# Performance work log

Hardware: AMD Instinct MI355X
Metric: run time of the kernel (lower is better)

The kernel has to match this reference:

```python
import jax, jax.numpy as jnp
import numpy as np

H = 256            # hidden_size
N_NODE = 50000     # item vocab
NUM_GRAPHS = 4096
NODES_PER_G = 20
EDGES_PER_G = 40
N = NUM_GRAPHS * NODES_PER_G      # 81920
E = NUM_GRAPHS * EDGES_PER_G      # 163840


def setup_inputs() -> dict:
    key = jax.random.key(0)
    ks = jax.random.split(key, 16)
    stdv = 1.0 / np.sqrt(H)
    u = lambda k, shape: jax.random.uniform(k, shape, jnp.float32, -stdv, stdv)

    # graph data: 1-based item ids, sorted batch vector, within-graph edges
    x = jax.random.randint(ks[0], (N,), 1, N_NODE, dtype=jnp.int64)
    batch = jnp.repeat(jnp.arange(NUM_GRAPHS, dtype=jnp.int64), NODES_PER_G)
    base = jnp.repeat(jnp.arange(NUM_GRAPHS, dtype=jnp.int64) * NODES_PER_G, EDGES_PER_G)
    src = base + jax.random.randint(ks[1], (E,), 0, NODES_PER_G, dtype=jnp.int64)
    dst = base + jax.random.randint(ks[2], (E,), 0, NODES_PER_G, dtype=jnp.int64)
    edge_index = jnp.stack([src, dst])

    return {
        "x": x, "edge_index": edge_index, "batch": batch,
        "emb": u(ks[3], (N_NODE, H)),
        "gated_w": u(ks[4], (2, H, H)),      # GatedGraphConv weight, num_layers=2
        "w_ih": u(ks[5], (3 * H, H)), "w_hh": u(ks[6], (3 * H, H)),
        "b_ih": u(ks[7], (3 * H,)), "b_hh": u(ks[8], (3 * H,)),
        "W1": u(ks[9], (H, H)), "b1": u(ks[10], (H,)),
        "W2": u(ks[11], (H, H)), "b2": u(ks[12], (H,)),
        "qw": u(ks[13], (1, H)), "qb": u(ks[14], (1,)),
        "W3": u(ks[15], (H, 2 * H)), "b3": jnp.zeros((H,), jnp.float32),
    }


def _forward(x, edge_index, batch, emb, gated_w, w_ih, w_hh, b_ih, b_hh,
             W1, b1, W2, b2, qw, qb, W3, b3):
    h = emb[x - 1]                                   # [N, H] embedding lookup
    src, dst = edge_index[0], edge_index[1]

    # GatedGraphConv: 2 layers of (linear -> scatter-add over edges -> GRUCell)
    for i in range(2):
        m = h @ gated_w[i]                           # [N, H]
        agg = jnp.zeros_like(h).at[dst].add(m[src])  # message aggregation
        gi = agg @ w_ih.T + b_ih                     # GRU input gates
        gh = h @ w_hh.T + b_hh                       # GRU hidden gates
        i_r, i_z, i_n = jnp.split(gi, 3, axis=-1)
        h_r, h_z, h_n = jnp.split(gh, 3, axis=-1)
        r = jax.nn.sigmoid(i_r + h_r)
        z = jax.nn.sigmoid(i_z + h_z)
        n = jnp.tanh(i_n + r * h_n)
        h = (1.0 - z) * n + z * h

    # Embedding2Score: last-node attention readout per graph
    counts = jnp.bincount(batch, length=NUM_GRAPHS)          # [B]
    last_idx = jnp.cumsum(counts) - 1                        # last node of each graph
    v_n = h[last_idx]                                        # [B, H]
    alpha = jax.nn.sigmoid(v_n[batch] @ W1.T + b1 + h @ W2.T + b2) @ qw.T + qb  # [N, 1]
    s_g = jax.ops.segment_sum(alpha * h, batch, num_segments=NUM_GRAPHS)        # [B, H]
    s_h = jnp.concatenate([v_n, s_g], axis=-1) @ W3.T + b3                      # [B, H]
    return s_h @ emb.T                                       # [B, N_NODE] scores


def reference(x, edge_index, batch, emb, gated_w, w_ih, w_hh, b_ih, b_hh,
              W1, b1, W2, b2, qw, qb, W3, b3):
    return _forward(x, edge_index, batch, emb, gated_w, w_ih, w_hh, b_ih, b_hh,
                    W1, b1, W2, b2, qw, qb, W3, b3)
```

## Files before the change

### kernel.cpp

```cpp
#include <hip/hip_runtime.h>

typedef __attribute__((ext_vector_type(8))) __bf16 bf16x8;
typedef __attribute__((ext_vector_type(4))) float f32x4;

#define DEV __device__ __forceinline__

DEV unsigned short f2bf(float f) {
  unsigned u = __float_as_uint(f);
  u = (u + 0x7fffu + ((u >> 16) & 1u)) >> 16;
  return (unsigned short)u;
}
DEV float bf2f(unsigned short s) { return __uint_as_float(((unsigned)s) << 16); }
DEV float sigm(float x) { return 1.f / (1.f + expf(-x)); }

DEV uint4 pack8(f32x4 a, f32x4 b) {
  uint4 o;
  o.x = (unsigned)f2bf(a[0]) | ((unsigned)f2bf(a[1]) << 16);
  o.y = (unsigned)f2bf(a[2]) | ((unsigned)f2bf(a[3]) << 16);
  o.z = (unsigned)f2bf(b[0]) | ((unsigned)f2bf(b[1]) << 16);
  o.w = (unsigned)f2bf(b[2]) | ((unsigned)f2bf(b[3]) << 16);
  return o;
}

#define GL16(SRC, LDSB)                                                                    \
  __builtin_amdgcn_global_load_lds(                                                       \
      (const __attribute__((address_space(1))) unsigned int*)(SRC),                       \
      (__attribute__((address_space(3))) unsigned int*)(LDSB), 16, 0, 0)

template<int MODE, bool BIAS>
__global__ __launch_bounds__(256)
void gemm_bt(const unsigned short* __restrict__ A, const unsigned short* __restrict__ Bm,
             const float* __restrict__ bias, void* __restrict__ Cv,
             const float* __restrict__ vw1, const float* __restrict__ qwf,
             const int* __restrict__ batchp, int M, int N, int K)
{
  __shared__ unsigned short sm[16384];
  unsigned short* As = sm;
  unsigned short* Bs = sm + 8192;

  const int tid  = threadIdx.x;
  const int lane = tid & 63;
  const int wv   = tid >> 6;
  const int wr   = (wv >> 1) << 6;
  const int wc   = (wv & 1) << 6;
  const long mTile = (long)blockIdx.y << 7;
  const long nTile = (long)blockIdx.x << 7;

  const f32x4 z4 = {0.f, 0.f, 0.f, 0.f};
  f32x4 acc[4][4];
  #pragma unroll
  for (int i = 0; i < 4; ++i)
    #pragma unroll
    for (int j = 0; j < 4; ++j) acc[i][j] = z4;

  const int crow = lane >> 3;
  const int ckb  = (lane & 7) << 4;

  for (int k0 = 0; k0 < K; k0 += 64) {
    #pragma unroll
    for (int i = 0; i < 4; ++i) {
      const int c   = (wv << 2) + i;
      const int row = (c << 3) + crow;
      const int kb  = ckb ^ ((row & 7) << 4);
      const unsigned short* sA = A + (mTile + row) * K + k0 + (kb >> 1);
      GL16(sA, (char*)As + (c << 10));
      int bn = (int)nTile + row; bn = bn < N ? bn : (N - 1);
      const unsigned short* sB = Bm + (long)bn * K + k0 + (kb >> 1);
      GL16(sB, (char*)Bs + (c << 10));
    }
    __syncthreads();
    #pragma unroll
    for (int kk = 0; kk < 64; kk += 32) {
      const int kbl = (kk + ((lane >> 4) << 3)) << 1;
      bf16x8 af[4], bfv[4];
      #pragma unroll
      for (int mi = 0; mi < 4; ++mi) {
        const int rr = wr + (mi << 4) + (lane & 15);
        af[mi] = *(const bf16x8*)((const char*)As + (rr << 7) + (kbl ^ ((rr & 7) << 4)));
      }
      #pragma unroll
      for (int ni = 0; ni < 4; ++ni) {
        const int rr = wc + (ni << 4) + (lane & 15);
        bfv[ni] = *(const bf16x8*)((const char*)Bs + (rr << 7) + (kbl ^ ((rr & 7) << 4)));
      }
      #pragma unroll
      for (int mi = 0; mi < 4; ++mi)
        #pragma unroll
        for (int ni = 0; ni < 4; ++ni)
          acc[mi][ni] = __builtin_amdgcn_mfma_f32_16x16x32_bf16(af[mi], bfv[ni], acc[mi][ni], 0, 0, 0);
    }
    __syncthreads();
  }

  if constexpr (MODE == 2) {
    const int slice = (int)blockIdx.x * 2 + (wc >> 6);
    #pragma unroll
    for (int mi = 0; mi < 4; ++mi) {
      #pragma unroll
      for (int j = 0; j < 4; ++j) {
        const long row = mTile + wr + (mi << 4) + ((lane >> 4) << 2) + j;
        const long vb = (long)batchp[row] << 8;
        float part = 0.f;
        #pragma unroll
        for (int ni = 0; ni < 4; ++ni) {
          const int col = (int)nTile + wc + (ni << 4) + (lane & 15);
          part += sigm(acc[mi][ni][j] + vw1[vb + col]) * qwf[col];
        }
        #pragma unroll
        for (int off = 1; off < 16; off <<= 1) part += __shfl_xor(part, off, 64);
        if ((lane & 15) == 0) ((float*)Cv)[(long)slice * M + row] = part;
      }
    }
  } else {
    #pragma unroll
    for (int ni = 0; ni < 4; ++ni) {
      const long col = nTile + wc + (ni << 4) + (lane & 15);
      if (col < N) {
        float bv = 0.f;
        if constexpr (BIAS) bv = bias[col];
        #pragma unroll
        for (int mi = 0; mi < 4; ++mi) {
          const long row = mTile + wr + (mi << 4) + ((lane >> 4) << 2);
          #pragma unroll
          for (int j = 0; j < 4; ++j) {
            const float v = acc[mi][ni][j] + bv;
            if constexpr (MODE == 1) ((unsigned short*)Cv)[(row + j) * N + col] = f2bf(v);
            else                     ((float*)Cv)[(row + j) * N + col] = v;
          }
        }
      }
    }
  }
}

__global__ __launch_bounds__(512, 2)
void k_ggru(const unsigned short* __restrict__ agg, const unsigned short* __restrict__ hin,
            const unsigned short* __restrict__ wpb, const unsigned short* __restrict__ whhb,
            const float* __restrict__ bih, const float* __restrict__ bhh,
            unsigned short* __restrict__ hout)
{
  extern __shared__ unsigned short sm[];
  const int tid  = threadIdx.x;
  const int lane = tid & 63;
  const int wv   = tid >> 6;
  const int rh   = wv >> 2;
  const int cg   = wv & 3;
  const int D0   = blockIdx.x << 6;
  const long mTile = (long)blockIdx.y << 7;

  const f32x4 z4 = {0.f, 0.f, 0.f, 0.f};
  f32x4 acc[4][6];
  #pragma unroll
  for (int i = 0; i < 4; ++i)
    #pragma unroll
    for (int g = 0; g < 6; ++g) acc[i][g] = z4;

  const int crow = lane >> 3;
  const int ckb  = (lane & 7) << 4;

  for (int k0 = 0; k0 < 256; k0 += 64) {
    #pragma unroll
    for (int i = 0; i < 10; ++i) {
      const int c = wv * 10 + i;
      if (c < 32) {
        const unsigned short* src = (c < 16) ? agg : hin;
        const int row = ((c & 15) << 3) + crow;
        const int kb  = ckb ^ ((row & 7) << 4);
        GL16(src + (mTile + row) * 256 + k0 + (kb >> 1), (char*)sm + (c << 10));
      } else {
        const int g  = (c - 32) >> 3;
        const int lr = (((c - 32) & 7) << 3) + crow;
        const unsigned short* Ws = (g < 3) ? wpb : whhb;
        const long grow = (long)((g % 3) * 256 + D0 + lr);
        const int kb = ckb ^ ((lr & 7) << 4);
        GL16(Ws + grow * 256 + k0 + (kb >> 1), (char*)sm + (c << 10));
      }
    }
    __syncthreads();
    #pragma unroll
    for (int kk = 0; kk < 64; kk += 32) {
      const int kbl = (kk + ((lane >> 4) << 3)) << 1;
      bf16x8 fa[4], fh[4], fb[6];
      #pragma unroll
      for (int mi = 0; mi < 4; ++mi) {
        const int r = (rh << 6) + (mi << 4) + (lane & 15);
        const int off = (r << 7) + (kbl ^ ((r & 7) << 4));
        fa[mi] = *(const bf16x8*)((const char*)sm + off);
        fh[mi] = *(const bf16x8*)((const char*)sm + 16384 + off);
      }
      const int lr = (cg << 4) + (lane & 15);
      const int boff = (lr << 7) + (kbl ^ ((lr & 7) << 4));
      #pragma unroll
      for (int g = 0; g < 6; ++g)
        fb[g] = *(const bf16x8*)((const char*)sm + 32768 + (g << 13) + boff);
      #pragma unroll
      for (int mi = 0; mi < 4; ++mi) {
        #pragma unroll
        for (int g = 0; g < 3; ++g)
          acc[mi][g] = __builtin_amdgcn_mfma_f32_16x16x32_bf16(fa[mi], fb[g], acc[mi][g], 0, 0, 0);
        #pragma unroll
        for (int g = 3; g < 6; ++g)
          acc[mi][g] = __builtin_amdgcn_mfma_f32_16x16x32_bf16(fh[mi], fb[g], acc[mi][g], 0, 0, 0);
      }
    }
    __syncthreads();
  }

  const int d = D0 + (cg << 4) + (lane & 15);
  const float bir = bih[d], biz = bih[256 + d], bin_ = bih[512 + d];
  const float bhr = bhh[d], bhz = bhh[256 + d], bhn  = bhh[512 + d];
  #pragma unroll
  for (int mi = 0; mi < 4; ++mi) {
    #pragma unroll
    for (int j = 0; j < 4; ++j) {
      const long row = mTile + (rh << 6) + (mi << 4) + ((lane >> 4) << 2) + j;
      const float hold = bf2f(hin[row * 256 + d]);
      const float r  = sigm(acc[mi][0][j] + bir + acc[mi][3][j] + bhr);
      const float z  = sigm(acc[mi][1][j] + biz + acc[mi][4][j] + bhz);
      const float n  = tanhf(acc[mi][2][j] + bin_ + r * (acc[mi][5][j] + bhn));
      hout[row * 256 + d] = f2bf((1.f - z) * n + z * hold);
    }
  }
}

__global__ void k_pre(const int* __restrict__ x, const float* __restrict__ emb,
                      unsigned short* __restrict__ embb, unsigned short* __restrict__ h,
                      const float* __restrict__ wih, const float* __restrict__ whh,
                      const float* __restrict__ W1, const float* __restrict__ W2,
                      const float* __restrict__ W3, const float* __restrict__ b1,
                      const float* __restrict__ b2, const float* __restrict__ gw,
                      unsigned short* __restrict__ wihb, unsigned short* __restrict__ whhb,
                      unsigned short* __restrict__ w1b, unsigned short* __restrict__ w2b,
                      unsigned short* __restrict__ w3b, float* __restrict__ b12,
                      unsigned short* __restrict__ gwb, int V8, int Nn8)
{
  const int b = blockIdx.x, t = threadIdx.x;
  if (b < V8) {
    const long i = (long)b * 256 + t;
    const f32x4 a = *(const f32x4*)(emb + i * 8);
    const f32x4 c = *(const f32x4*)(emb + i * 8 + 4);
    *(uint4*)(embb + i * 8) = pack8(a, c);
  } else if (b < V8 + Nn8) {
    const long i = (long)(b - V8) * 256 + t;
    const long node = i >> 5;
    const int  d0 = ((int)i & 31) << 3;
    const long row = (long)x[node] - 1;
    const float* p = emb + row * 256 + d0;
    const f32x4 a = *(const f32x4*)p;
    const f32x4 c = *(const f32x4*)(p + 4);
    *(uint4*)(h + node * 256 + d0) = pack8(a, c);
  } else {
    const int bw = b - V8 - Nn8;
    const float* src; unsigned short* dst; long base;
    if (bw < 96)       { src = wih; dst = wihb; base = bw; }
    else if (bw < 192) { src = whh; dst = whhb; base = bw - 96; }
    else if (bw < 224) { src = W1;  dst = w1b;  base = bw - 192; }
    else if (bw < 256) { src = W2;  dst = w2b;  base = bw - 224; }
    else if (bw < 320) { src = W3;  dst = w3b;  base = bw - 256; }
    else if (bw == 320) { b12[t] = b1[t] + b2[t]; return; }
    else               { src = gw;  dst = gwb;  base = bw - 321; }
    const long i = base * 256 + t;
    const f32x4 a = *(const f32x4*)(src + i * 8);
    const f32x4 c = *(const f32x4*)(src + i * 8 + 4);
    *(uint4*)(dst + i * 8) = pack8(a, c);
  }
}

__global__ void k_scatter(const unsigned short* __restrict__ m, const int* __restrict__ ei,
                          unsigned short* __restrict__ agg, int E)
{
  __shared__ float aggs[20 * 256];
  __shared__ int es[40], ed[40];
  const int g = blockIdx.x;
  const int d = threadIdx.x;
  if (d < 40) es[d] = ei[g * 40 + d];
  if (d >= 128 && d < 168) ed[d - 128] = ei[E + g * 40 + (d - 128)];
  #pragma unroll
  for (int i = 0; i < 20; ++i) aggs[i * 256 + d] = 0.f;
  __syncthreads();
  for (int e = 0; e < 40; ++e) {
    const float mv = bf2f(m[(long)es[e] * 256 + d]);
    const int loc = ed[e] - g * 20;
    aggs[loc * 256 + d] += mv;
  }
  const long base = (long)g * (20 * 256);
  #pragma unroll
  for (int i = 0; i < 20; ++i)
    agg[base + i * 256 + d] = f2bf(aggs[i * 256 + d]);
}

__global__ void k_vn(const unsigned short* __restrict__ h, const int* __restrict__ batch,
                     unsigned short* __restrict__ vn, unsigned short* __restrict__ cat, int n)
{
  const long i = (long)blockIdx.x * 256 + threadIdx.x;
  const long g = i >> 5;
  const int  d0 = ((int)i & 31) << 3;
  int lo = 0, hi = n;
  while (lo < hi) { const int mid = (lo + hi) >> 1; if (batch[mid] > (int)g) hi = mid; else lo = mid + 1; }
  const uint4 v = *(const uint4*)(h + (long)(lo - 1) * 256 + d0);
  *(uint4*)(vn + g * 256 + d0) = v;
  *(uint4*)(cat + g * 512 + d0) = v;
}

__global__ void k_sg(const float* __restrict__ alph2, const float* __restrict__ qb,
                     const unsigned short* __restrict__ h, unsigned short* __restrict__ cat, int Nn)
{
  __shared__ float al[20];
  const int g = blockIdx.x, d = threadIdx.x;
  if (d < 20) {
    const int n = g * 20 + d;
    al[d] = qb[0] + alph2[n] + alph2[Nn + n] + alph2[2 * Nn + n] + alph2[3 * Nn + n];
  }
  __syncthreads();
  float s = 0.f;
  const unsigned short* hp = h + (long)g * 20 * 256 + d;
  #pragma unroll
  for (int i = 0; i < 20; ++i) s += al[i] * bf2f(hp[i * 256]);
  cat[(long)g * 512 + 256 + d] = f2bf(s);
}

extern "C" void kernel_launch(void* const* d_in, const int* in_sizes, int n_in,
                              void* d_out, int out_size, void* d_ws, size_t ws_size,
                              hipStream_t stream)
{
  const int*   x     = (const int*)  d_in[0];
  const int*   ei    = (const int*)  d_in[1];
  const int*   batch = (const int*)  d_in[2];
  const float* emb   = (const float*)d_in[3];
  const float* gw    = (const float*)d_in[4];
  const float* wih   = (const float*)d_in[5];
  const float* whh   = (const float*)d_in[6];
  const float* bih   = (const float*)d_in[7];
  const float* bhh   = (const float*)d_in[8];
  const float* W1    = (const float*)d_in[9];
  const float* b1    = (const float*)d_in[10];
  const float* W2    = (const float*)d_in[11];
  const float* b2    = (const float*)d_in[12];
  const float* qw    = (const float*)d_in[13];
  const float* qb    = (const float*)d_in[14];
  const float* W3    = (const float*)d_in[15];
  const float* b3    = (const float*)d_in[16];

  const int Nn = in_sizes[0];
  const int E  = in_sizes[1] / 2;
  const int V  = in_sizes[3] / 256;
  const int B  = out_size / V;

  char* w = (char*)d_ws;
  auto take = [&](size_t bytes) { char* r = w; w += (bytes + 1023) & ~(size_t)1023; return r; };
  unsigned short* h_   = (unsigned short*)take((size_t)Nn * 256 * 2);
  unsigned short* m_   = (unsigned short*)take((size_t)Nn * 256 * 2);
  unsigned short* agg_ = (unsigned short*)take((size_t)Nn * 256 * 2);
  unsigned short* embb = (unsigned short*)take((size_t)V * 256 * 2);
  unsigned short* gwb  = (unsigned short*)take((size_t)2 * 65536 * 2);
  unsigned short* wihb = (unsigned short*)take((size_t)768 * 256 * 2);
  unsigned short* whhb = (unsigned short*)take((size_t)768 * 256 * 2);
  unsigned short* wp0  = (unsigned short*)take((size_t)768 * 256 * 2);
  unsigned short* wp1  = (unsigned short*)take((size_t)768 * 256 * 2);
  unsigned short* w1b  = (unsigned short*)take((size_t)65536 * 2);
  unsigned short* w2b  = (unsigned short*)take((size_t)65536 * 2);
  unsigned short* w3b  = (unsigned short*)take((size_t)131072 * 2);
  unsigned short* vnb  = (unsigned short*)take((size_t)B * 256 * 2);
  unsigned short* catb = (unsigned short*)take((size_t)B * 512 * 2);
  unsigned short* shb  = (unsigned short*)take((size_t)B * 256 * 2);
  float*          b12  = (float*)take(256 * 4);
  float*          alph2= (float*)take((size_t)4 * Nn * 4);
  float*          vw1  = (float*)take((size_t)B * 256 * 4);

  const int MBn = Nn / 128;
  const int MBb = B / 128;
  const int NBv = (V + 127) / 128;
  const int V8  = V / 8;
  const int Nn8 = Nn / 8;

  k_pre<<<dim3(V8 + Nn8 + 385), 256, 0, stream>>>(x, emb, embb, h_,
      wih, whh, W1, W2, W3, b1, b2, gw, wihb, whhb, w1b, w2b, w3b, b12, gwb, V8, Nn8);

  gemm_bt<1, false><<<dim3(2, 6), 256, 0, stream>>>(wihb, gwb, nullptr, wp0,
                                                    nullptr, nullptr, nullptr, 768, 256, 256);
  gemm_bt<1, false><<<dim3(2, 6), 256, 0, stream>>>(wihb, gwb + 65536, nullptr, wp1,
                                                    nullptr, nullptr, nullptr, 768, 256, 256);

  unsigned short* hc = h_;
  unsigned short* mb = m_;
  for (int L = 0; L < 2; ++L) {
    k_scatter<<<dim3(B), 256, 0, stream>>>(hc, ei, agg_, E);
    k_ggru<<<dim3(4, MBn), 512, 81920, stream>>>(agg_, hc, (L == 0 ? wp0 : wp1), whhb,
                                                 bih, bhh, mb);
    unsigned short* t = hc; hc = mb; mb = t;
  }

  k_vn<<<dim3(B * 32 / 256), 256, 0, stream>>>(hc, batch, vnb, catb, Nn);
  gemm_bt<0, true><<<dim3(2, MBb), 256, 0, stream>>>(vnb, w1b, b12, vw1,
                                                     nullptr, nullptr, nullptr, B, 256, 256);
  gemm_bt<2, false><<<dim3(2, MBn), 256, 0, stream>>>(hc, w2b, nullptr, alph2,
                                                      vw1, qw, batch, Nn, 256, 256);
  k_sg<<<dim3(B), 256, 0, stream>>>(alph2, qb, hc, catb, Nn);
  gemm_bt<1, true><<<dim3(2, MBb), 256, 0, stream>>>(catb, w3b, b3, shb,
                                                     nullptr, nullptr, nullptr, B, 256, 512);

  gemm_bt<0, false><<<dim3(NBv, MBb), 256, 0, stream>>>(shb, embb, nullptr, (float*)d_out,
                                                        nullptr, nullptr, nullptr, B, V, 256);

  (void)n_in; (void)ws_size;
}
```

Before: 761.2 us.

## Double-buffer LDS tiles in bf16 GEMM to overlap global loads with MFMA

Doubles the shared-memory buffer and issues the next K-tile's global_load_lds into the alternate buffer before computing on the current one. It waits with a partial vmcnt so only the current tile's loads must be complete. This hides global-to-LDS latency behind MFMA work. In exchange, doubling LDS use to 64KB per block may lower occupancy, and the hand-written waitcnt and barrier ordering is fragile.

```diff
diff --git a/kernel.cpp b/kernel.cpp
--- a/kernel.cpp
+++ b/kernel.cpp
@@ -34,9 +34,7 @@
              const float* __restrict__ vw1, const float* __restrict__ qwf,
              const int* __restrict__ batchp, int M, int N, int K)
 {
-  __shared__ unsigned short sm[16384];
-  unsigned short* As = sm;
-  unsigned short* Bs = sm + 8192;
+  __shared__ unsigned short sm[32768];
 
   const int tid  = threadIdx.x;
   const int lane = tid & 63;
@@ -56,19 +54,35 @@
   const int crow = lane >> 3;
   const int ckb  = (lane & 7) << 4;
 
-  for (int k0 = 0; k0 < K; k0 += 64) {
+  auto stage = [&](int buf, int k0) {
+    char* base = (char*)sm + (buf << 15);
     #pragma unroll
     for (int i = 0; i < 4; ++i) {
       const int c   = (wv << 2) + i;
       const int row = (c << 3) + crow;
       const int kb  = ckb ^ ((row & 7) << 4);
       const unsigned short* sA = A + (mTile + row) * K + k0 + (kb >> 1);
-      GL16(sA, (char*)As + (c << 10));
+      GL16(sA, base + (c << 10));
       int bn = (int)nTile + row; bn = bn < N ? bn : (N - 1);
       const unsigned short* sB = Bm + (long)bn * K + k0 + (kb >> 1);
-      GL16(sB, (char*)Bs + (c << 10));
-    }
-    __syncthreads();
+      GL16(sB, base + 16384 + (c << 10));
+    }
+  };
+
+  const int nt = K >> 6;
+  stage(0, 0);
+  int cur = 0;
+  for (int t = 0; t < nt; ++t) {
+    if (t + 1 < nt) {
+      stage(cur ^ 1, (t + 1) << 6);
+      asm volatile("s_waitcnt vmcnt(8)" ::: "memory");
+    } else {
+      asm volatile("s_waitcnt vmcnt(0)" ::: "memory");
+    }
+    __builtin_amdgcn_s_barrier();
+    asm volatile("" ::: "memory");
+    const char* As = (const char*)sm + (cur << 15);
+    const char* Bs = As + 16384;
     #pragma unroll
     for (int kk = 0; kk < 64; kk += 32) {
       const int kbl = (kk + ((lane >> 4) << 3)) << 1;
@@ -76,12 +90,12 @@
       #pragma unroll
       for (int mi = 0; mi < 4; ++mi) {
         const int rr = wr + (mi << 4) + (lane & 15);
-        af[mi] = *(const bf16x8*)((const char*)As + (rr << 7) + (kbl ^ ((rr & 7) << 4)));
+        af[mi] = *(const bf16x8*)(As + (rr << 7) + (kbl ^ ((rr & 7) << 4)));
       }
       #pragma unroll
       for (int ni = 0; ni < 4; ++ni) {
         const int rr = wc + (ni << 4) + (lane & 15);
-        bfv[ni] = *(const bf16x8*)((const char*)Bs + (rr << 7) + (kbl ^ ((rr & 7) << 4)));
+        bfv[ni] = *(const bf16x8*)(Bs + (rr << 7) + (kbl ^ ((rr & 7) << 4)));
       }
       #pragma unroll
       for (int mi = 0; mi < 4; ++mi)
@@ -89,7 +103,9 @@
         for (int ni = 0; ni < 4; ++ni)
           acc[mi][ni] = __builtin_amdgcn_mfma_f32_16x16x32_bf16(af[mi], bfv[ni], acc[mi][ni], 0, 0, 0);
     }
-    __syncthreads();
+    asm volatile("" ::: "memory");
+    __builtin_amdgcn_s_barrier();
+    cur ^= 1;
   }
 
   if constexpr (MODE == 2) {
```

New measurement: 738.2 us. 3.0% less time.
